# Performance work log

Hardware: AMD Instinct MI355X
Metric: run time of the kernel (lower is better)

## Reference

```python
import jax, jax.numpy as jnp
from jax import lax
import numpy as np

EMBED = 256; MDIM = 256; DSTATE = 128; DCONV = 4
NHEADS = 8; HEADDIM = 64; DINNER = 512            # expand=2 -> d_inner=512; headdim 64 -> 8 heads
CONVDIM = DINNER + 2 * DSTATE                      # 768: conv runs over x,B,C channels
DINPROJ = 2 * DINNER + 2 * DSTATE + NHEADS         # 1288
B = 4; H = 64; W = 64; L = H * W

def _ln(x, g, b, eps=1e-5):
    mu = x.mean(-1, keepdims=True)
    v = ((x - mu) ** 2).mean(-1, keepdims=True)
    return (x - mu) / jnp.sqrt(v + eps) * g + b

def _bn(x, g, b, m, v, eps=1e-5):  # x: (B,C,H,W); eval-mode BatchNorm2d
    return (x - m[:, None, None]) / jnp.sqrt(v[:, None, None] + eps) * g[:, None, None] + b[:, None, None]

def _mamba_branch(seq, ln_g, ln_b, in_W, in_b, cw, cb, A_log, Dh, dt_bias, norm_g, out_W, out_b):
    # Pre-LN Mamba2 block with residual. seq: (B, L, MDIM)
    bsz, slen, _ = seq.shape
    x = _ln(seq, ln_g, ln_b)
    zxbcdt = x @ in_W.T + in_b                                   # (B,L,DINPROJ)
    z = zxbcdt[..., :DINNER]
    xBC = zxbcdt[..., DINNER:DINNER + CONVDIM]
    dt = zxbcdt[..., DINNER + CONVDIM:]                          # (B,L,NHEADS)
    # depthwise causal conv1d over sequence dim
    xc = lax.conv_general_dilated(xBC.transpose(0, 2, 1), cw[:, None, :], (1,),
                                  [(DCONV - 1, 0)], feature_group_count=CONVDIM)
    xBC = jax.nn.silu(xc.transpose(0, 2, 1) + cb)
    xh = xBC[..., :DINNER].reshape(bsz, slen, NHEADS, HEADDIM)
    Bm = xBC[..., DINNER:DINNER + DSTATE]                        # (B,L,N)
    Cm = xBC[..., DINNER + DSTATE:]                              # (B,L,N)
    dt = jax.nn.softplus(dt + dt_bias)                           # (B,L,H)
    dA = jnp.exp(dt * (-jnp.exp(A_log)))                         # (B,L,H)
    dtx = dt[..., None] * xh                                     # (B,L,H,P)
    def step(h, inp):
        dA_t, dtx_t, B_t, C_t = inp
        h = h * dA_t[:, :, None, None] + dtx_t[..., None] * B_t[:, None, None, :]
        return h, jnp.einsum('bhpn,bn->bhp', h, C_t)
    h0 = jnp.zeros((bsz, NHEADS, HEADDIM, DSTATE), seq.dtype)
    xs = (dA.transpose(1, 0, 2), dtx.transpose(1, 0, 2, 3),
          Bm.transpose(1, 0, 2), Cm.transpose(1, 0, 2))
    _, ys = lax.scan(step, h0, xs)                               # (L,B,H,P)
    y = ys.transpose(1, 0, 2, 3) + Dh[None, None, :, None] * xh
    y = y.reshape(bsz, slen, DINNER) * jax.nn.silu(z)            # gate
    y = y / jnp.sqrt((y ** 2).mean(-1, keepdims=True) + 1e-5) * norm_g  # RMSNormGated
    return seq + (y @ out_W.T + out_b)

def _forward(curr_bev, prev_bev, conv3_w, bn3_g, bn3_b, bn3_m, bn3_v, conv1_w, bn1_g, bn1_b, bn1_m, bn1_v, fuse_W, fuse_b, ln_g, ln_b, inp_W, inp_b, m_ln_g, m_ln_b, m_in_W, m_in_b, conv_w, conv_b, A_log, Dp, dt_bias, m_norm_g, m_out_W, m_out_b, outp_W, outp_b, bev_h, bev_w):
    b, l, c = curr_bev.shape
    curr = curr_bev.reshape(b, bev_h, bev_w, c)
    prev = prev_bev.reshape(b, bev_h, bev_w, c)  # delta_yaw is None -> no alignment
    cat = jnp.concatenate([curr, prev], -1).transpose(0, 3, 1, 2)         # (B,2C,H,W)
    b3 = _bn(lax.conv_general_dilated(cat, conv3_w, (1, 1), [(1, 1), (1, 1)]), bn3_g, bn3_b, bn3_m, bn3_v)
    b1 = _bn(lax.conv_general_dilated(cat, conv1_w, (1, 1), [(0, 0), (0, 0)]), bn1_g, bn1_b, bn1_m, bn1_v)
    z = jax.nn.relu(jnp.concatenate([b3, b1], 1)).transpose(0, 2, 3, 1)   # (B,H,W,C)
    z = _ln(z @ fuse_W.T + fuse_b, ln_g, ln_b)
    fl = z.reshape(b, l, c)                                               # row-major forward
    fu = z.transpose(0, 2, 1, 3).reshape(b, l, c)                         # column-major forward
    seqs = jnp.stack([fl, fu, fl[:, ::-1], fu[:, ::-1]], 0)               # (4,B,L,C)
    def branch(seq, iW, ib, lg, lb, mW, mb, cw, cb, al, dh, db, ng, oW, ob, pW, pb):
        s = seq @ iW.T + ib
        s = _mamba_branch(s, lg, lb, mW, mb, cw, cb, al, dh, db, ng, oW, ob)
        return s @ pW.T + pb
    outs = jax.vmap(branch)(seqs, inp_W, inp_b, m_ln_g, m_ln_b, m_in_W, m_in_b, conv_w, conv_b, A_log, Dp, dt_bias, m_norm_g, m_out_W, m_out_b, outp_W, outp_b)
    ofl = outs[0].reshape(b, bev_h, bev_w, c)
    ofu = outs[1].reshape(b, bev_w, bev_h, c).transpose(0, 2, 1, 3)
    orl = outs[2][:, ::-1].reshape(b, bev_h, bev_w, c)
    oru = outs[3][:, ::-1].reshape(b, bev_w, bev_h, c).transpose(0, 2, 1, 3)
    fused = 0.25 * (ofl + ofu + orl + oru)
    return curr_bev + fused.reshape(b, l, c)  # resid dropout = identity at inference

def setup_inputs() -> dict:
    key = jax.random.key(0)
    ks = jax.random.split(key, 16)
    rn = lambda k, s, sc=0.02: jax.random.normal(k, s, jnp.float32) * sc
    return {
        "curr_bev": jax.random.normal(ks[0], (B, L, EMBED), jnp.float32),
        "prev_bev": jax.random.normal(ks[1], (B, L, EMBED), jnp.float32),
        "conv3_w": rn(ks[2], (EMBED // 2, 2 * EMBED, 3, 3)),
        "bn3_g": jnp.ones((EMBED // 2,)), "bn3_b": jnp.zeros((EMBED // 2,)),
        "bn3_m": jnp.zeros((EMBED // 2,)), "bn3_v": jnp.ones((EMBED // 2,)),
        "conv1_w": rn(ks[3], (EMBED // 2, 2 * EMBED, 1, 1)),
        "bn1_g": jnp.ones((EMBED // 2,)), "bn1_b": jnp.zeros((EMBED // 2,)),
        "bn1_m": jnp.zeros((EMBED // 2,)), "bn1_v": jnp.ones((EMBED // 2,)),
        "fuse_W": rn(ks[4], (EMBED, EMBED)), "fuse_b": jnp.zeros((EMBED,)),
        "ln_g": jnp.ones((EMBED,)), "ln_b": jnp.zeros((EMBED,)),
        "inp_W": rn(ks[5], (4, MDIM, EMBED)), "inp_b": jnp.zeros((4, MDIM)),
        "m_ln_g": jnp.ones((4, MDIM)), "m_ln_b": jnp.zeros((4, MDIM)),
        "m_in_W": rn(ks[6], (4, DINPROJ, MDIM)), "m_in_b": jnp.zeros((4, DINPROJ)),
        "conv_w": rn(ks[7], (4, CONVDIM, DCONV), 0.1), "conv_b": jnp.zeros((4, CONVDIM)),
        "A_log": jnp.tile(jnp.log(jnp.arange(1, NHEADS + 1, dtype=jnp.float32)), (4, 1)),
        "Dp": jnp.ones((4, NHEADS)),
        "dt_bias": rn(ks[8], (4, NHEADS), 0.1),
        "m_norm_g": jnp.ones((4, DINNER)),
        "m_out_W": rn(ks[9], (4, MDIM, DINNER)), "m_out_b": jnp.zeros((4, MDIM)),
        "outp_W": rn(ks[10], (4, EMBED, MDIM)), "outp_b": jnp.zeros((4, EMBED)),
        "bev_h": H, "bev_w": W,
    }

def reference(curr_bev, prev_bev, conv3_w, bn3_g, bn3_b, bn3_m, bn3_v, conv1_w, bn1_g, bn1_b, bn1_m, bn1_v, fuse_W, fuse_b, ln_g, ln_b, inp_W, inp_b, m_ln_g, m_ln_b, m_in_W, m_in_b, conv_w, conv_b, A_log, Dp, dt_bias, m_norm_g, m_out_W, m_out_b, outp_W, outp_b, bev_h, bev_w):
    return _forward(curr_bev, prev_bev, conv3_w, bn3_g, bn3_b, bn3_m, bn3_v, conv1_w, bn1_g, bn1_b, bn1_m, bn1_v, fuse_W, fuse_b, ln_g, ln_b, inp_W, inp_b, m_ln_g, m_ln_b, m_in_W, m_in_b, conv_w, conv_b, A_log, Dp, dt_bias, m_norm_g, m_out_W, m_out_b, outp_W, outp_b, bev_h, bev_w)
```

## Files before the change

kernel.cpp:

```cpp
#include <hip/hip_runtime.h>
#include <hip/hip_bf16.h>
#include <cstdint>
#include <cstddef>

typedef unsigned short u16;
typedef unsigned int u32;
typedef __attribute__((ext_vector_type(8))) __bf16 bfx8;
typedef __attribute__((ext_vector_type(4))) float f32x4;

static __device__ __forceinline__ float bitf(u32 v){ float f; __builtin_memcpy(&f,&v,4); return f; }
static __device__ __forceinline__ float bf2f(u16 v){ return bitf(((u32)v)<<16); }
static __device__ __forceinline__ u16 f2bf(float f){ __bf16 b=(__bf16)f; u16 r; __builtin_memcpy(&r,&b,2); return r; }
static __device__ __forceinline__ u32 pk2(float a,float b){ return (u32)f2bf(a) | ((u32)f2bf(b)<<16); }
static __device__ __forceinline__ void unpk8(uint4 r, float* o){
  o[0]=bitf(r.x<<16); o[1]=bitf(r.x&0xffff0000u);
  o[2]=bitf(r.y<<16); o[3]=bitf(r.y&0xffff0000u);
  o[4]=bitf(r.z<<16); o[5]=bitf(r.z&0xffff0000u);
  o[6]=bitf(r.w<<16); o[7]=bitf(r.w&0xffff0000u);
}
static __device__ __forceinline__ void unpk4(uint2 r, float* o){
  o[0]=bitf(r.x<<16); o[1]=bitf(r.x&0xffff0000u);
  o[2]=bitf(r.y<<16); o[3]=bitf(r.y&0xffff0000u);
}
static __device__ __forceinline__ void async16(void* lds, const void* g){
  __builtin_amdgcn_global_load_lds((const __attribute__((address_space(1))) u32*)g,
                                   (__attribute__((address_space(3))) u32*)lds, 16, 0, 0);
}

struct GemmArgs {
  const u16* A; long aZ; int lda;
  const u16* Bw; long bZ; int ldb;
  const float* bias; int biasZ;
  const float* scale; const float* shift;
  const u16* add; long addZ;
  u16* C; long cZ; int ldc; int colOff;
  int K;
  const u16* pad;
  int dirBase;
};

template<int AMODE, int EPI>
__global__ __launch_bounds__(256)
void gemm_bt(GemmArgs g)
{
  __shared__ u16 smA[128*64];
  __shared__ u16 smB[128*64];
  const int tid = threadIdx.x;
  const int l = tid & 63;
  const int wv = tid >> 6;
  const int wr = wv >> 1, wc = wv & 1;
  const int z = blockIdx.z;
  const int r0 = blockIdx.x * 128;
  const int n0 = blockIdx.y * 128;

  const u16* Abase = g.A + (size_t)z * g.aZ;
  const u16* Bbase = g.Bw + (size_t)z * g.bZ;
  const int ldb = g.ldb ? g.ldb : g.K;

  f32x4 acc[4][4];
  #pragma unroll
  for (int i=0;i<4;i++)
    #pragma unroll
    for (int j=0;j<4;j++) acc[i][j] = (f32x4){0.f,0.f,0.f,0.f};

  const int nkt = g.K >> 6;
  #pragma unroll 1
  for (int kt=0; kt<nkt; ++kt) {
    const int k0 = kt << 6;
    #pragma unroll
    for (int it=0; it<4; ++it) {
      const int s = it*256 + tid;
      const int row = s >> 3, ch = s & 7;
      const u16* ga;
      if (AMODE == 0) {
        ga = Abase + (size_t)(r0+row) * g.lda + k0 + ch*8;
      } else if (AMODE == 1) {
        int rr = r0 + row; int li = rr & 4095; int bb = rr >> 12;
        int dir = g.dirBase + z;
        int l2 = (dir & 2) ? (4095 - li) : li;
        int sl = (dir & 1) ? (((l2 & 63) << 6) | (l2 >> 6)) : l2;
        ga = Abase + (size_t)((bb << 12) | sl) * g.lda + k0 + ch*8;
      } else if (AMODE == 2) {
        int rr = r0 + row; int bb = rr >> 12; int li = rr & 4095;
        int yy = li >> 6, xx = li & 63;
        int tap = z, kin = k0;
        int dy = tap / 3 - 1, dx = tap % 3 - 1;
        ga = g.pad + (((size_t)(bb*66 + yy+dy+1))*66 + (xx+dx+1))*512 + kin + ch*8;
      } else {
        int rr = r0 + row; int bb = rr >> 12; int li = rr & 4095;
        int yy = li >> 6, xx = li & 63;
        ga = g.pad + (((size_t)(bb*66 + yy+1))*66 + (xx+1))*512 + k0 + ch*8;
      }
      async16(&smA[(size_t)(it*256 + (tid & ~63))*8], ga);
      const u16* gb = Bbase + (size_t)(n0+row) * ldb + k0 + ch*8;
      async16(&smB[(size_t)(it*256 + (tid & ~63))*8], gb);
    }
    __syncthreads();
    #pragma unroll
    for (int kk=0; kk<2; ++kk) {
      bfx8 av[4], bv[4];
      #pragma unroll
      for (int mi=0; mi<4; ++mi) {
        int ra = wr*64 + mi*16 + (l & 15);
        av[mi] = *(const bfx8*)&smA[ra*64 + kk*32 + (l>>4)*8];
      }
      #pragma unroll
      for (int ni=0; ni<4; ++ni) {
        int rb = wc*64 + ni*16 + (l & 15);
        bv[ni] = *(const bfx8*)&smB[rb*64 + kk*32 + (l>>4)*8];
      }
      #pragma unroll
      for (int mi=0; mi<4; ++mi)
        #pragma unroll
        for (int ni=0; ni<4; ++ni)
          acc[mi][ni] = __builtin_amdgcn_mfma_f32_16x16x32_bf16(av[mi], bv[ni], acc[mi][ni], 0, 0, 0);
    }
    __syncthreads();
  }

  const float* bias_d = (EPI == 0 || EPI == 3) ? g.bias + (size_t)z * g.biasZ : nullptr;
  const u16* add_d = (EPI == 3) ? g.add + (size_t)z * g.addZ : nullptr;
  u16* Cd = g.C + (size_t)z * g.cZ;
  float* Cf = (float*)g.C + (size_t)z * g.cZ;
  #pragma unroll
  for (int mi=0; mi<4; ++mi) {
    #pragma unroll
    for (int ni=0; ni<4; ++ni) {
      f32x4 v = acc[mi][ni];
      const int gr = r0 + wr*64 + mi*16 + ((l >> 4) << 2);
      const int gc = n0 + wc*64 + ni*16 + (l & 15);
      #pragma unroll
      for (int q=0; q<4; ++q) {
        const int r = gr + q;
        float x = v[q];
        if (EPI == 2) {
          x = fmaxf(fmaf(x, g.scale[gc], g.shift[gc]), 0.f);
          Cd[(size_t)r * g.ldc + g.colOff + gc] = f2bf(x);
        } else if (EPI == 3) {
          x += bias_d[gc] + bf2f(add_d[(size_t)r * g.ldc + gc]);
          Cd[(size_t)r * g.ldc + g.colOff + gc] = f2bf(x);
        } else if (EPI == 4) {
          Cf[(size_t)r * g.ldc + g.colOff + gc] = x;
        } else {
          x += bias_d[gc];
          Cd[(size_t)r * g.ldc + g.colOff + gc] = f2bf(x);
        }
      }
    }
  }
}

__global__ void castk(const float* __restrict__ s, u16* __restrict__ d, int n)
{
  int i = (blockIdx.x*256 + threadIdx.x)*4;
  if (i < n){
    float4 v = *(const float4*)(s+i);
    ushort4 o; o.x=f2bf(v.x); o.y=f2bf(v.y); o.z=f2bf(v.z); o.w=f2bf(v.w);
    *(ushort4*)(d+i) = o;
  }
}

__global__ void c3rep(const float* __restrict__ w, u16* __restrict__ o)
{
  int id = blockIdx.x*256 + threadIdx.x;
  int oc = id / 4608, rem = id % 4608;
  int tap = rem >> 9, ic = rem & 511;
  o[id] = f2bf(w[((size_t)oc*512 + ic)*9 + tap]);
}

__global__ void bnssk(const float* g3,const float* b3,const float* m3,const float* v3,
                      const float* g1,const float* b1,const float* m1,const float* v1,
                      float* out)
{
  int t = threadIdx.x; int i = t & 127;
  if (t < 128){ float sc = g3[i]*rsqrtf(v3[i]+1e-5f); out[i]=sc; out[128+i]=b3[i]-m3[i]*sc; }
  else        { float sc = g1[i]*rsqrtf(v1[i]+1e-5f); out[256+i]=sc; out[384+i]=b1[i]-m1[i]*sc; }
}

__global__ __launch_bounds__(256)
void c3red(const float* __restrict__ P, const float* __restrict__ bnss, u16* __restrict__ zin)
{
  const int id = blockIdx.x*256 + threadIdx.x;
  const size_t base = (size_t)id * 4;
  const int r = (int)(base >> 7), c = (int)(base & 127);
  float4 s = {0.f,0.f,0.f,0.f};
  #pragma unroll
  for (int z=0; z<9; ++z){
    float4 v = *(const float4*)(P + (size_t)z*2097152 + base);
    s.x += v.x; s.y += v.y; s.z += v.z; s.w += v.w;
  }
  float4 sc = *(const float4*)(bnss + c);
  float4 sh = *(const float4*)(bnss + 128 + c);
  ushort4 o;
  o.x = f2bf(fmaxf(fmaf(s.x, sc.x, sh.x), 0.f));
  o.y = f2bf(fmaxf(fmaf(s.y, sc.y, sh.y), 0.f));
  o.z = f2bf(fmaxf(fmaf(s.z, sc.z, sh.z), 0.f));
  o.w = f2bf(fmaxf(fmaf(s.w, sc.w, sh.w), 0.f));
  *(ushort4*)(zin + (size_t)r*256 + c) = o;
}

__global__ __launch_bounds__(256)
void padk(const float* __restrict__ curr, const float* __restrict__ prev, u16* __restrict__ pad)
{
  const int id = blockIdx.x*256 + threadIdx.x;
  const int c8 = id & 63;
  int t = id >> 6;
  const int xx = t % 66; t /= 66;
  const int yy = t % 66; const int b = t / 66;
  const int c0 = c8*8;
  uint4 o;
  if (yy==0 || yy==65 || xx==0 || xx==65){ o.x=0;o.y=0;o.z=0;o.w=0; }
  else {
    const int l = (yy-1)*64 + (xx-1);
    const float* s = (c0 < 256) ? curr + ((size_t)b*4096 + l)*256 + c0
                                : prev + ((size_t)b*4096 + l)*256 + (c0-256);
    float4 a = *(const float4*)s, bb = *(const float4*)(s+4);
    o.x = pk2(a.x,a.y); o.y = pk2(a.z,a.w); o.z = pk2(bb.x,bb.y); o.w = pk2(bb.z,bb.w);
  }
  *(uint4*)(pad + (((size_t)b*66 + yy)*66 + xx)*512 + c0) = o;
}

__global__ __launch_bounds__(256)
void ln256(const u16* __restrict__ in, long inZ, u16* __restrict__ out, long outZ,
           const float* __restrict__ gw, const float* __restrict__ bw, int pz)
{
  const int z = blockIdx.z;
  const int row = blockIdx.x*4 + (threadIdx.x>>6);
  const int l = threadIdx.x & 63;
  const u16* ip = in + (size_t)z*inZ + (size_t)row*256 + l*4;
  ushort4 rr = *(const ushort4*)ip;
  float v0=bf2f(rr.x), v1=bf2f(rr.y), v2=bf2f(rr.z), v3=bf2f(rr.w);
  float s = v0+v1+v2+v3;
  float ss = v0*v0+v1*v1+v2*v2+v3*v3;
  #pragma unroll
  for(int m=1;m<64;m<<=1){ s += __shfl_xor(s,m); ss += __shfl_xor(ss,m); }
  float mu = s*(1.f/256.f);
  float var = ss*(1.f/256.f) - mu*mu;
  float rs = rsqrtf(var + 1e-5f);
  const float* g = gw + (size_t)z*pz; const float* b = bw + (size_t)z*pz;
  int c = l*4;
  u16* op = out + (size_t)z*outZ + (size_t)row*256 + c;
  ushort4 o; o.x=f2bf((v0-mu)*rs*g[c]+b[c]); o.y=f2bf((v1-mu)*rs*g[c+1]+b[c+1]);
  o.z=f2bf((v2-mu)*rs*g[c+2]+b[c+2]); o.w=f2bf((v3-mu)*rs*g[c+3]+b[c+3]);
  *(ushort4*)op = o;
}

__global__ __launch_bounds__(256)
void rms512(u16* __restrict__ Y, const float* __restrict__ gw)
{
  const int z = blockIdx.z;
  const int row = blockIdx.x*4 + (threadIdx.x>>6);
  const int l = threadIdx.x & 63;
  u16* p = Y + ((size_t)z*16384 + row)*512 + l*8;
  uint4 raw = *(const uint4*)p;
  float v[8]; unpk8(raw, v);
  float ss = 0.f;
  #pragma unroll
  for (int j=0;j<8;j++) ss += v[j]*v[j];
  #pragma unroll
  for (int m=1;m<64;m<<=1) ss += __shfl_xor(ss, m);
  const float sc = rsqrtf(ss*(1.f/512.f) + 1e-5f);
  const float* g = gw + (size_t)z*512 + l*8;
  uint4 o;
  o.x = pk2(v[0]*sc*g[0], v[1]*sc*g[1]);
  o.y = pk2(v[2]*sc*g[2], v[3]*sc*g[3]);
  o.z = pk2(v[4]*sc*g[4], v[5]*sc*g[5]);
  o.w = pk2(v[6]*sc*g[6], v[7]*sc*g[7]);
  *(uint4*)p = o;
}

__global__ __launch_bounds__(256)
void dtk(const u16* __restrict__ xln, const float* __restrict__ minW,
         const float* __restrict__ minB, const float* __restrict__ dtb,
         float* __restrict__ DT)
{
  __shared__ float sx[32*257];
  const int z = blockIdx.z;
  const int r0 = blockIdx.x * 32;
  const int tid = threadIdx.x;
  {
    const int rr = tid >> 3, cc = (tid & 7) * 32;
    const u16* src = xln + ((size_t)z*16384 + r0 + rr)*256 + cc;
    #pragma unroll
    for (int q=0;q<4;q++){
      uint4 raw = *(const uint4*)(src + q*8);
      float v[8]; unpk8(raw, v);
      #pragma unroll
      for (int j=0;j<8;j++) sx[rr*257 + cc + q*8 + j] = v[j];
    }
  }
  __syncthreads();
  const int ri = tid >> 3, hv = tid & 7;
  const float* wrow = minW + ((size_t)z*1288 + 1280 + hv)*256;
  float acc = 0.f;
  #pragma unroll 4
  for (int k=0; k<256; k+=4){
    float4 wq = *(const float4*)(wrow + k);
    acc += sx[ri*257+k]*wq.x + sx[ri*257+k+1]*wq.y + sx[ri*257+k+2]*wq.z + sx[ri*257+k+3]*wq.w;
  }
  acc += minB[(size_t)z*1288 + 1280 + hv] + dtb[z*8 + hv];
  float dt = (acc > 20.f) ? acc : log1pf(expf(acc));
  DT[((size_t)z*16384 + r0 + ri)*8 + hv] = dt;
}

__global__ __launch_bounds__(256)
void cak(const float* __restrict__ DT, float* __restrict__ CA,
         const float* __restrict__ alog, int dirBase)
{
  const int z = blockIdx.z;
  const int gidx = blockIdx.x*4 + (threadIdx.x>>6);
  const int lane = threadIdx.x & 63;
  const int c = gidx & 63, bh = gidx >> 6;
  const int b = bh >> 3, hh = bh & 7;
  const size_t row = (size_t)z*16384 + (size_t)b*4096 + c*64 + lane;
  float x = DT[row*8 + hh];
  #pragma unroll
  for (int m=1;m<64;m<<=1){ float o = __shfl_up(x, m); if (lane >= m) x += o; }
  float eA = expf(alog[(dirBase+z)*8 + hh]);
  CA[row*8 + hh] = -eA * x;
}

__global__ __launch_bounds__(256)
void convbc(const u16* __restrict__ xbcr, u16* __restrict__ bcc,
            const float* __restrict__ cw, const float* __restrict__ cb)
{
  __shared__ float cwS[4][256];
  __shared__ float cbS[256];
  const int tid = threadIdx.x;
  const int id = blockIdx.x*256 + tid;
  const int c8 = id & 31;
  const int r = (id >> 5) & 16383;
  const int d = id >> 19;
  {
    float4 w4 = *(const float4*)(cw + ((size_t)d*768 + 512 + tid)*4);
    cwS[0][tid]=w4.x; cwS[1][tid]=w4.y; cwS[2][tid]=w4.z; cwS[3][tid]=w4.w;
    cbS[tid] = cb[(size_t)d*768 + 512 + tid];
  }
  __syncthreads();
  const int li = r & 4095;
  const int col = 512 + c8*8;
  const u16* base = xbcr + (size_t)d*16777216 + (size_t)(r - li)*768 + col;
  float acc[8];
  #pragma unroll
  for (int j=0;j<8;j++) acc[j] = cbS[c8*8+j];
  #pragma unroll
  for (int tap=0; tap<4; ++tap){
    int lt = li - 3 + tap;
    if (lt >= 0){
      uint4 raw = *(const uint4*)(base + (size_t)lt*768);
      float v[8]; unpk8(raw, v);
      #pragma unroll
      for (int j=0;j<8;j++)
        acc[j] = fmaf(v[j], cwS[tap][c8*8+j], acc[j]);
    }
  }
  uint4 o;
  float s[8];
  #pragma unroll
  for (int j=0;j<8;j++) s[j] = acc[j] / (1.f + __expf(-acc[j]));
  o.x = pk2(s[0],s[1]); o.y = pk2(s[2],s[3]); o.z = pk2(s[4],s[5]); o.w = pk2(s[6],s[7]);
  *(uint4*)(bcc + ((size_t)d*16384 + r)*256 + c8*8) = o;
}

__global__ __launch_bounds__(256)
void convx(const u16* __restrict__ xbcr, u16* __restrict__ xct,
           const float* __restrict__ cw, const float* __restrict__ cb)
{
  __shared__ u16 T[128*72];
  __shared__ float cwX[4][128];
  __shared__ float cbX[128];
  const int bx = blockIdx.x, z = blockIdx.z;
  const int pq = bx & 3, c = (bx>>2) & 63, b = bx >> 8;
  const int tid = threadIdx.x;
  const u16* xb = xbcr + (size_t)z*16777216 + (size_t)b*4096*768;
  if (tid < 128){
    float4 w4 = *(const float4*)(cw + (size_t)z*3072 + (pq*128+tid)*4);
    cwX[0][tid]=w4.x; cwX[1][tid]=w4.y; cwX[2][tid]=w4.z; cwX[3][tid]=w4.w;
    cbX[tid] = cb[z*768 + pq*128 + tid];
  }
  __syncthreads();
  #pragma unroll
  for (int u=0; u<4; ++u){
    int idx = u*256 + tid;
    int s = idx >> 4, seg = idx & 15;
    int li = c*64 + s;
    int col = pq*128 + seg*8;
    float acc[8];
    #pragma unroll
    for (int j=0;j<8;j++) acc[j] = cbX[seg*8+j];
    #pragma unroll
    for (int tap=0; tap<4; ++tap){
      int lt = li - 3 + tap;
      if (lt >= 0){
        uint4 raw = *(const uint4*)(xb + (size_t)lt*768 + col);
        float v[8]; unpk8(raw, v);
        #pragma unroll
        for (int j=0;j<8;j++) acc[j] = fmaf(v[j], cwX[tap][seg*8+j], acc[j]);
      }
    }
    #pragma unroll
    for (int j=0;j<8;j++)
      T[(seg*8+j)*72 + s] = f2bf(acc[j] / (1.f + __expf(-acc[j])));
  }
  __syncthreads();
  #pragma unroll
  for (int u=0; u<4; ++u){
    int idx = u*256 + tid;
    int pl = idx >> 3, sg = idx & 7;
    uint4 v = *(const uint4*)&T[pl*72 + sg*8];
    *(uint4*)(xct + (size_t)z*8388608 + (size_t)(pq*128+pl)*16384 + b*4096 + c*64 + sg*8) = v;
  }
}

__global__ __launch_bounds__(256)
void btk(const u16* __restrict__ bcc, u16* __restrict__ bt)
{
  __shared__ u16 T[128*72];
  const int bx = blockIdx.x, z = blockIdx.z;
  const int c = bx & 63, b = bx >> 6;
  const int tid = threadIdx.x;
  const u16* src = bcc + ((size_t)z*16384 + (size_t)b*4096 + c*64)*256;
  #pragma unroll
  for (int u=0; u<4; ++u){
    int idx = u*256 + tid;
    int s = idx >> 4, seg = idx & 15;
    uint4 raw = *(const uint4*)(src + (size_t)s*256 + seg*8);
    u16 t8[8]; *(uint4*)t8 = raw;
    #pragma unroll
    for (int j=0;j<8;j++) T[(seg*8+j)*72 + s] = t8[j];
  }
  __syncthreads();
  #pragma unroll
  for (int u=0; u<4; ++u){
    int idx = u*256 + tid;
    int n = idx >> 3, sg = idx & 7;
    uint4 v = *(const uint4*)&T[n*72 + sg*8];
    *(uint4*)(bt + (size_t)z*2097152 + (size_t)n*16384 + b*4096 + c*64 + sg*8) = v;
  }
}

__global__ __launch_bounds__(256)
void csk(const u16* __restrict__ xct, const u16* __restrict__ bt,
         const float* __restrict__ DT, const float* __restrict__ CA,
         u16* __restrict__ CS)
{
  __shared__ u16 Xw[128*72];
  __shared__ u16 Bt[128*72];
  __shared__ float wS[64*2];
  const int bx = blockIdx.x, z = blockIdx.z;
  const int pq = bx & 3, c = (bx>>2) & 63, b = bx >> 8;
  const int tid = threadIdx.x, l = tid & 63, w = tid >> 6;
  const size_t rowb = (size_t)z*16384 + (size_t)b*4096;
  const int p0 = pq*128;
  if (tid < 128){
    int s = tid & 63, hi = tid >> 6;
    int hh = pq*2 + hi;
    float ca63 = CA[(rowb + c*64 + 63)*8 + hh];
    float cav  = CA[(rowb + c*64 + s)*8 + hh];
    float dtv  = DT[(rowb + c*64 + s)*8 + hh];
    wS[s*2+hi] = __expf(ca63 - cav) * dtv;
  }
  __syncthreads();
  #pragma unroll
  for (int u=0; u<4; ++u){
    int idx = u*256 + tid;
    int pl = idx >> 3, sg = idx & 7;
    int hi = pl >> 6;
    uint4 raw = *(const uint4*)(xct + (size_t)z*8388608 + (size_t)(p0+pl)*16384 + b*4096 + c*64 + sg*8);
    float v[8]; unpk8(raw, v);
    uint4 o;
    o.x = pk2(v[0]*wS[(sg*8+0)*2+hi], v[1]*wS[(sg*8+1)*2+hi]);
    o.y = pk2(v[2]*wS[(sg*8+2)*2+hi], v[3]*wS[(sg*8+3)*2+hi]);
    o.z = pk2(v[4]*wS[(sg*8+4)*2+hi], v[5]*wS[(sg*8+5)*2+hi]);
    o.w = pk2(v[6]*wS[(sg*8+6)*2+hi], v[7]*wS[(sg*8+7)*2+hi]);
    *(uint4*)&Xw[pl*72 + sg*8] = o;
  }
  #pragma unroll
  for (int u=0; u<4; ++u){
    int idx = u*256 + tid;
    int n = idx >> 3, sg = idx & 7;
    *(uint4*)&Bt[n*72 + sg*8] =
      *(const uint4*)(bt + (size_t)z*2097152 + (size_t)n*16384 + b*4096 + c*64 + sg*8);
  }
  __syncthreads();
  f32x4 acc[8][2];
  #pragma unroll
  for (int i=0;i<8;i++)
    #pragma unroll
    for (int j=0;j<2;j++) acc[i][j] = (f32x4){0.f,0.f,0.f,0.f};
  #pragma unroll
  for (int kk=0; kk<2; ++kk){
    bfx8 bvp[2];
    #pragma unroll
    for (int ni=0; ni<2; ++ni)
      bvp[ni] = *(const bfx8*)&Xw[(w*32 + ni*16 + (l&15))*72 + kk*32 + (l>>4)*8];
    #pragma unroll
    for (int mi=0; mi<8; ++mi){
      bfx8 av = *(const bfx8*)&Bt[(mi*16 + (l&15))*72 + kk*32 + (l>>4)*8];
      #pragma unroll
      for (int ni=0; ni<2; ++ni)
        acc[mi][ni] = __builtin_amdgcn_mfma_f32_16x16x32_bf16(av, bvp[ni], acc[mi][ni], 0, 0, 0);
    }
  }
  #pragma unroll
  for (int mi=0; mi<8; ++mi){
    #pragma unroll
    for (int ni=0; ni<2; ++ni){
      int gp = p0 + w*32 + ni*16 + (l&15);
      int bhx = b*8 + (gp>>6); int pin = gp & 63;
      int n0 = mi*16 + ((l>>4)<<2);
      u32* cp = (u32*)&CS[(size_t)z*16777216 + (size_t)bhx*524288 + (size_t)c*8192 + (size_t)pin*128 + n0];
      cp[0] = pk2(acc[mi][ni][0], acc[mi][ni][1]);
      cp[1] = pk2(acc[mi][ni][2], acc[mi][ni][3]);
    }
  }
}

__global__ __launch_bounds__(256)
void combk(const u16* __restrict__ CS, const float* __restrict__ CA,
           u16* __restrict__ H)
{
  __shared__ float aL[64];
  const int bx = blockIdx.x;
  const int z = blockIdx.z;
  const int nh = bx & 1, pg = (bx >> 1) & 3, bh = bx >> 3;
  const int b = bh >> 3, hh = bh & 7;
  const int tid = threadIdx.x;
  const int p = pg*16 + (tid >> 4), n = nh*64 + (tid & 15)*4;
  const size_t rowb = (size_t)z*16384 + (size_t)b*4096;
  if (tid < 64) aL[tid] = __expf(CA[(rowb + tid*64 + 63)*8 + hh]);
  __syncthreads();
  const u16* Cs = CS + (size_t)z*16777216 + (size_t)bh*524288 + (size_t)p*128 + n;
  u16* Hd = H + (size_t)z*16777216 + (size_t)bh*524288 + (size_t)p*128 + n;
  float h[4];
  #pragma unroll
  for (int j=0;j<4;j++) h[j]=0.f;
  uint2 pf = *(const uint2*)Cs;
  #pragma unroll 1
  for (int c=0; c<64; ++c){
    uint2 cur = pf;
    if (c < 63) pf = *(const uint2*)(Cs + (size_t)(c+1)*8192);
    uint2 o;
    o.x = pk2(h[0],h[1]); o.y = pk2(h[2],h[3]);
    *(uint2*)(Hd + (size_t)c*8192) = o;
    float v[4]; unpk4(cur, v);
    const float a = aL[c];
    #pragma unroll
    for (int j=0;j<4;j++) h[j] = fmaf(h[j], a, v[j]);
  }
}

__global__ __launch_bounds__(256)
void yk2(const u16* __restrict__ bcc, const u16* __restrict__ xct,
         const float* __restrict__ DT, const float* __restrict__ CA,
         const u16* __restrict__ H, const float* __restrict__ Dp,
         u16* __restrict__ Y)
{
  __shared__ u16 Bs[64*136];
  __shared__ u16 Hs[64*136];
  __shared__ u16 Xt[64*72];
  __shared__ u16 Sm[64*72];
  __shared__ float caL[64], dtL[64];
  const int bx = blockIdx.x, z = blockIdx.z;
  const int c = bx & 63, bh = bx >> 6;
  const int b = bh >> 3, hh = bh & 7;
  const int tid = threadIdx.x, l = tid & 63, w = tid >> 6;
  const size_t rowb = (size_t)z*16384 + (size_t)b*4096;
  const u16* bcp = bcc + (rowb + c*64)*256;
  const u16* Hd = H + (size_t)z*16777216 + (size_t)bh*524288 + (size_t)c*8192;
  const u16* xcp = xct + (size_t)z*8388608 + (size_t)(hh*64)*16384 + b*4096 + c*64;
  const float Dh = Dp[z*8 + hh];

  bfx8 av[4];
  #pragma unroll
  for (int kk=0; kk<4; ++kk)
    av[kk] = *(const bfx8*)(bcp + (size_t)(w*16 + (l&15))*256 + 128 + kk*32 + (l>>4)*8);

  if (tid < 64){
    caL[tid] = CA[(rowb + c*64 + tid)*8 + hh];
    dtL[tid] = DT[(rowb + c*64 + tid)*8 + hh];
  }
  #pragma unroll
  for (int u=0; u<4; ++u){
    int idx = u*256 + tid; int s = idx >> 4, sg = idx & 15;
    *(uint4*)&Bs[s*136 + sg*8] = *(const uint4*)(bcp + (size_t)s*256 + sg*8);
  }
  #pragma unroll
  for (int u=0; u<4; ++u){
    int idx = u*256 + tid; int p = idx >> 4, sg = idx & 15;
    *(uint4*)&Hs[p*136 + sg*8] = *(const uint4*)(Hd + (size_t)p*128 + sg*8);
  }
  #pragma unroll
  for (int u=0; u<2; ++u){
    int idx = u*256 + tid; int p = idx >> 3, sg = idx & 7;
    *(uint4*)&Xt[p*72 + sg*8] = *(const uint4*)(xcp + (size_t)p*16384 + sg*8);
  }
  __syncthreads();

  f32x4 sacc[4], acc2[4];
  #pragma unroll
  for (int i=0;i<4;i++){ sacc[i] = (f32x4){0.f,0.f,0.f,0.f}; acc2[i] = (f32x4){0.f,0.f,0.f,0.f}; }
  #pragma unroll
  for (int kk=0; kk<4; ++kk){
    #pragma unroll
    for (int st=0; st<4; ++st){
      bfx8 bv = *(const bfx8*)&Bs[(st*16 + (l&15))*136 + kk*32 + (l>>4)*8];
      sacc[st] = __builtin_amdgcn_mfma_f32_16x16x32_bf16(av[kk], bv, sacc[st], 0, 0, 0);
      bfx8 hv = *(const bfx8*)&Hs[(st*16 + (l&15))*136 + kk*32 + (l>>4)*8];
      acc2[st] = __builtin_amdgcn_mfma_f32_16x16x32_bf16(av[kk], hv, acc2[st], 0, 0, 0);
    }
  }
  #pragma unroll
  for (int st=0; st<4; ++st){
    #pragma unroll
    for (int q=0;q<4;q++){
      int t = w*16 + (l>>4)*4 + q;
      int s = st*16 + (l&15);
      float m = (s <= t) ? __expf(caL[t]-caL[s]) * dtL[s] : 0.f;
      Sm[t*72 + s] = f2bf(sacc[st][q] * m);
    }
  }
  #pragma unroll
  for (int pt=0; pt<4; ++pt)
    #pragma unroll
    for (int q=0;q<4;q++){
      int t = w*16 + (l>>4)*4 + q;
      acc2[pt][q] *= __expf(caL[t]);
    }
  __syncthreads();
  #pragma unroll
  for (int kk=0; kk<2; ++kk){
    bfx8 sv = *(const bfx8*)&Sm[(w*16 + (l&15))*72 + kk*32 + (l>>4)*8];
    #pragma unroll
    for (int pt=0; pt<4; ++pt){
      bfx8 bv = *(const bfx8*)&Xt[(pt*16 + (l&15))*72 + kk*32 + (l>>4)*8];
      acc2[pt] = __builtin_amdgcn_mfma_f32_16x16x32_bf16(sv, bv, acc2[pt], 0, 0, 0);
    }
  }
  u16* Yrow = Y + (rowb + c*64)*512 + hh*64;
  #pragma unroll
  for (int pt=0; pt<4; ++pt){
    #pragma unroll
    for (int q=0;q<4;q++){
      int t = w*16 + (l>>4)*4 + q;
      int p = pt*16 + (l&15);
      float xv = bf2f(Xt[p*72 + t]);
      float zf = bf2f(Yrow[(size_t)t*512 + p]);
      float yv = (acc2[pt][q] + Dh*xv) * (zf/(1.f+__expf(-zf)));
      Yrow[(size_t)t*512 + p] = f2bf(yv);
    }
  }
}

__global__ __launch_bounds__(256)
void finalk(const float* __restrict__ curr, const u16* __restrict__ outs, float* __restrict__ o)
{
  const int row = blockIdx.x*4 + (threadIdx.x>>6);
  const int c4 = (threadIdx.x & 63)*4;
  const int b = row >> 12, li = row & 4095;
  const int T = ((li & 63) << 6) | (li >> 6);
  const size_t rb = (size_t)b*4096;
  const ushort4 a0 = *(const ushort4*)(outs + (size_t)0*4194304 + ((rb+li)*256 + c4));
  const ushort4 a1 = *(const ushort4*)(outs + (size_t)1*4194304 + ((rb+T)*256 + c4));
  const ushort4 a2 = *(const ushort4*)(outs + (size_t)2*4194304 + ((rb+4095-li)*256 + c4));
  const ushort4 a3 = *(const ushort4*)(outs + (size_t)3*4194304 + ((rb+4095-T)*256 + c4));
  float4 cv = *(const float4*)(curr + (size_t)row*256 + c4);
  float4 r;
  r.x = cv.x + 0.25f*(bf2f(a0.x)+bf2f(a1.x)+bf2f(a2.x)+bf2f(a3.x));
  r.y = cv.y + 0.25f*(bf2f(a0.y)+bf2f(a1.y)+bf2f(a2.y)+bf2f(a3.y));
  r.z = cv.z + 0.25f*(bf2f(a0.z)+bf2f(a1.z)+bf2f(a2.z)+bf2f(a3.z));
  r.w = cv.w + 0.25f*(bf2f(a0.w)+bf2f(a1.w)+bf2f(a2.w)+bf2f(a3.w));
  *(float4*)(o + (size_t)row*256 + c4) = r;
}

extern "C" void kernel_launch(void* const* d_in, const int* in_sizes, int n_in,
                              void* d_out, int out_size, void* d_ws, size_t ws_size,
                              hipStream_t stream)
{
  (void)in_sizes; (void)n_in; (void)out_size;
  const float* curr   = (const float*)d_in[0];
  const float* prev   = (const float*)d_in[1];
  const float* conv3w = (const float*)d_in[2];
  const float* bn3g=(const float*)d_in[3], *bn3b=(const float*)d_in[4], *bn3m=(const float*)d_in[5], *bn3v=(const float*)d_in[6];
  const float* conv1w = (const float*)d_in[7];
  const float* bn1g=(const float*)d_in[8], *bn1b=(const float*)d_in[9], *bn1m=(const float*)d_in[10], *bn1v=(const float*)d_in[11];
  const float* fuseW=(const float*)d_in[12], *fuseB=(const float*)d_in[13];
  const float* lng=(const float*)d_in[14], *lnb=(const float*)d_in[15];
  const float* inpW=(const float*)d_in[16], *inpB=(const float*)d_in[17];
  const float* mlng=(const float*)d_in[18], *mlnb=(const float*)d_in[19];
  const float* minW=(const float*)d_in[20], *minB=(const float*)d_in[21];
  const float* cw=(const float*)d_in[22], *cb=(const float*)d_in[23];
  const float* alog=(const float*)d_in[24], *Dp=(const float*)d_in[25], *dtb=(const float*)d_in[26];
  const float* mng=(const float*)d_in[27];
  const float* moutW=(const float*)d_in[28], *moutB=(const float*)d_in[29];
  const float* outpW=(const float*)d_in[30], *outpB=(const float*)d_in[31];

  char* ws = (char*)d_ws;
  size_t off = 0;
  auto alloc = [&](size_t bytes){ size_t o = off; off = (off + bytes + 1023) & ~(size_t)1023; return o; };
  const size_t O_WFUSE = alloc((size_t)256*256*2);
  const size_t O_WINP  = alloc((size_t)4*256*256*2);
  const size_t O_WMIN  = alloc((size_t)4*1288*256*2);
  const size_t O_WMOUT = alloc((size_t)4*256*512*2);
  const size_t O_WOUTP = alloc((size_t)4*256*256*2);
  const size_t O_WC3   = alloc((size_t)128*4608*2);
  const size_t O_WC1   = alloc((size_t)128*512*2);
  const size_t O_BNSS  = alloc(512*4);
  const size_t O_ZF    = alloc((size_t)16384*256*2);
  const size_t O_OUTS  = alloc((size_t)4*16384*256*2);
  const size_t O_P     = off;

  const size_t S0d  = (size_t)16384*256*2;
  const size_t XLNd = (size_t)16384*256*2;
  const size_t Yd   = (size_t)16384*512*2;
  const size_t XCTd = (size_t)512*16384*2;
  const size_t BTd  = (size_t)128*16384*2;
  const size_t DTd  = (size_t)16384*8*4;
  const size_t CAd  = (size_t)16384*8*4;
  const size_t XHd  = (size_t)16777216*2;
  const size_t perdir = S0d + XLNd + Yd + XCTd + BTd + DTd + CAd + XHd;

  const size_t PADsz = (size_t)4*66*66*512*2;
  const size_t CPsz  = (size_t)9*16384*128*4;
  const size_t PREsz = PADsz + CPsz + (size_t)16384*256*2*2 + 4096;

  int nd = 0;
  for (int cand = 4; cand >= 1; cand >>= 1) {
    size_t need = (size_t)cand*perdir; if (need < PREsz) need = PREsz;
    if (O_P + need <= ws_size) { nd = cand; break; }
  }
  if (nd == 0) return;

  #define WP(o) ((u16*)(ws + (o)))
  #define FP(o) ((float*)(ws + (o)))

  const size_t O_PAD = O_P;
  const size_t O_CP  = O_PAD + PADsz;
  const size_t O_ZIN = O_CP + CPsz;
  const size_t O_ZFT = O_ZIN + (size_t)16384*256*2;

  bnssk<<<1, 256, 0, stream>>>(bn3g,bn3b,bn3m,bn3v, bn1g,bn1b,bn1m,bn1v, FP(O_BNSS));
  castk<<<64, 256, 0, stream>>>(fuseW, WP(O_WFUSE), 65536);
  castk<<<256, 256, 0, stream>>>(inpW, WP(O_WINP), 262144);
  castk<<<1288, 256, 0, stream>>>(minW, WP(O_WMIN), 1318912);
  castk<<<512, 256, 0, stream>>>(moutW, WP(O_WMOUT), 524288);
  castk<<<256, 256, 0, stream>>>(outpW, WP(O_WOUTP), 262144);
  castk<<<64, 256, 0, stream>>>(conv1w, WP(O_WC1), 65536);
  c3rep<<<2304, 256, 0, stream>>>(conv3w, WP(O_WC3));
  padk<<<4356, 256, 0, stream>>>(curr, prev, WP(O_PAD));

  GemmArgs a;
  a = {}; a.A = WP(O_PAD); a.pad = WP(O_PAD);
  a.Bw = WP(O_WC3); a.bZ = 512; a.ldb = 4608;
  a.C = WP(O_CP); a.cZ = 2097152; a.ldc = 128; a.colOff = 0; a.K = 512;
  gemm_bt<2,4><<<dim3(128,1,9), 256, 0, stream>>>(a);
  c3red<<<2048, 256, 0, stream>>>(FP(O_CP), FP(O_BNSS), WP(O_ZIN));
  a = {}; a.A = WP(O_PAD); a.pad = WP(O_PAD); a.Bw = WP(O_WC1); a.bZ = 0; a.ldb = 512;
  a.scale = FP(O_BNSS)+256; a.shift = FP(O_BNSS)+384;
  a.C = WP(O_ZIN); a.cZ = 0; a.ldc = 256; a.colOff = 128; a.K = 512;
  gemm_bt<3,2><<<dim3(128,1,1), 256, 0, stream>>>(a);
  a = {}; a.A = WP(O_ZIN); a.aZ = 0; a.lda = 256; a.Bw = WP(O_WFUSE); a.bZ = 0; a.ldb = 256;
  a.bias = fuseB; a.biasZ = 0; a.C = WP(O_ZFT); a.cZ = 0; a.ldc = 256; a.colOff = 0; a.K = 256;
  gemm_bt<0,0><<<dim3(128,2,1), 256, 0, stream>>>(a);
  ln256<<<dim3(4096,1,1), 256, 0, stream>>>(WP(O_ZFT), 0, WP(O_ZF), 0, lng, lnb, 0);

  for (int d0 = 0; d0 < 4; d0 += nd) {
    size_t o = O_P;
    const size_t O_S0  = o; o += (size_t)nd*S0d;
    const size_t O_XLN = o; o += (size_t)nd*XLNd;
    const size_t O_Y   = o; o += (size_t)nd*Yd;
    const size_t O_XCT = o; o += (size_t)nd*XCTd;
    const size_t O_BT  = o; o += (size_t)nd*BTd;
    const size_t O_DT  = o; o += (size_t)nd*DTd;
    const size_t O_CA  = o; o += (size_t)nd*CAd;
    const size_t O_XH  = o;
    const size_t O_BCC = O_XLN;
    const size_t O_S1  = O_XLN;

    a = {}; a.A = WP(O_ZF); a.aZ = 0; a.lda = 256;
    a.Bw = WP(O_WINP) + (size_t)d0*65536; a.bZ = 65536; a.ldb = 256;
    a.bias = inpB + d0*256; a.biasZ = 256;
    a.C = WP(O_S0); a.cZ = 4194304; a.ldc = 256; a.colOff = 0; a.K = 256; a.dirBase = d0;
    gemm_bt<1,0><<<dim3(128,2,nd), 256, 0, stream>>>(a);
    ln256<<<dim3(4096,1,nd), 256, 0, stream>>>(WP(O_S0), 4194304, WP(O_XLN), 4194304,
                                               mlng + d0*256, mlnb + d0*256, 256);
    dtk<<<dim3(512,1,nd), 256, 0, stream>>>(WP(O_XLN), minW + (size_t)d0*329728,
                                            minB + d0*1288, dtb + d0*8, FP(O_DT));
    cak<<<dim3(512,1,nd), 256, 0, stream>>>(FP(O_DT), FP(O_CA), alog, d0);
    a = {}; a.A = WP(O_XLN); a.aZ = 4194304; a.lda = 256;
    a.Bw = WP(O_WMIN) + (size_t)d0*329728; a.bZ = 329728; a.ldb = 256;
    a.bias = minB + d0*1288; a.biasZ = 1288;
    a.C = WP(O_Y); a.cZ = 8388608; a.ldc = 512; a.colOff = 0; a.K = 256;
    gemm_bt<0,0><<<dim3(128,4,nd), 256, 0, stream>>>(a);
    a = {}; a.A = WP(O_XLN); a.aZ = 4194304; a.lda = 256;
    a.Bw = WP(O_WMIN) + (size_t)d0*329728 + (size_t)512*256; a.bZ = 329728; a.ldb = 256;
    a.bias = minB + d0*1288 + 512; a.biasZ = 1288;
    a.C = WP(O_XH); a.cZ = 16777216; a.ldc = 768; a.colOff = 0; a.K = 256;
    gemm_bt<0,0><<<dim3(128,6,nd), 256, 0, stream>>>(a);
    convbc<<<nd*2048, 256, 0, stream>>>(WP(O_XH), WP(O_BCC), cw + d0*3072, cb + d0*768);
    convx<<<dim3(1024,1,nd), 256, 0, stream>>>(WP(O_XH), WP(O_XCT), cw + d0*3072, cb + d0*768);
    btk<<<dim3(256,1,nd), 256, 0, stream>>>(WP(O_BCC), WP(O_BT));
    csk<<<dim3(1024,1,nd), 256, 0, stream>>>(WP(O_XCT), WP(O_BT), FP(O_DT), FP(O_CA), WP(O_XH));
    combk<<<dim3(256,1,nd), 256, 0, stream>>>(WP(O_XH), FP(O_CA), WP(O_XH));
    yk2<<<dim3(2048,1,nd), 256, 0, stream>>>(WP(O_BCC), WP(O_XCT), FP(O_DT), FP(O_CA),
                                             WP(O_XH), Dp + d0*8, WP(O_Y));
    rms512<<<dim3(4096,1,nd), 256, 0, stream>>>(WP(O_Y), mng + d0*512);
    a = {}; a.A = WP(O_Y); a.aZ = 8388608; a.lda = 512;
    a.Bw = WP(O_WMOUT) + (size_t)d0*131072; a.bZ = 131072; a.ldb = 512;
    a.bias = moutB + d0*256; a.biasZ = 256;
    a.add = WP(O_S0); a.addZ = 4194304;
    a.C = WP(O_S1); a.cZ = 4194304; a.ldc = 256; a.colOff = 0; a.K = 512;
    gemm_bt<0,3><<<dim3(128,2,nd), 256, 0, stream>>>(a);
    a = {}; a.A = WP(O_S1); a.aZ = 4194304; a.lda = 256;
    a.Bw = WP(O_WOUTP) + (size_t)d0*65536; a.bZ = 65536; a.ldb = 256;
    a.bias = outpB + d0*256; a.biasZ = 256;
    a.C = WP(O_OUTS) + (size_t)d0*4194304; a.cZ = 4194304; a.ldc = 256; a.colOff = 0; a.K = 256;
    gemm_bt<0,0><<<dim3(128,2,nd), 256, 0, stream>>>(a);
  }

  finalk<<<4096, 256, 0, stream>>>(curr, WP(O_OUTS), (float*)d_out);

  #undef WP
  #undef FP
}
```

Baseline: 730.7 us.

## Fold RMSNorm into out-proj GEMM and precompute C·B scores per chunk

The RMSNorm gain is folded into the bf16 out-projection weights, and the per-row rsqrt scale is applied in a new GEMM epilogue. The norm kernel now only writes one scale per row instead of rewriting the whole Y tensor. Separately, the intra-chunk C·Bᵀ score matrix is computed once per (batch, chunk) in a new kernel, not recomputed for each of the 8 heads inside yk2, which now loads the precomputed scores from memory. This trades redundant MFMA work for an extra kernel launch and global traffic, and the scores are rounded to bf16 before masking.

```diff
diff --git a/kernel.cpp b/kernel.cpp
--- a/kernel.cpp
+++ b/kernel.cpp
@@ -33,6 +33,7 @@
   const float* bias; int biasZ;
   const float* scale; const float* shift;
   const u16* add; long addZ;
+  const float* rowsc; long rowscZ;
   u16* C; long cZ; int ldc; int colOff;
   int K;
   const u16* pad;
@@ -118,8 +119,9 @@
     __syncthreads();
   }
 
-  const float* bias_d = (EPI == 0 || EPI == 3) ? g.bias + (size_t)z * g.biasZ : nullptr;
-  const u16* add_d = (EPI == 3) ? g.add + (size_t)z * g.addZ : nullptr;
+  const float* bias_d = (EPI == 0 || EPI == 3 || EPI == 5) ? g.bias + (size_t)z * g.biasZ : nullptr;
+  const u16* add_d = (EPI == 3 || EPI == 5) ? g.add + (size_t)z * g.addZ : nullptr;
+  const float* rowsc_d = (EPI == 5) ? g.rowsc + (size_t)z * g.rowscZ : nullptr;
   u16* Cd = g.C + (size_t)z * g.cZ;
   float* Cf = (float*)g.C + (size_t)z * g.cZ;
   #pragma unroll
@@ -139,6 +141,9 @@
         } else if (EPI == 3) {
           x += bias_d[gc] + bf2f(add_d[(size_t)r * g.ldc + gc]);
           Cd[(size_t)r * g.ldc + g.colOff + gc] = f2bf(x);
+        } else if (EPI == 5) {
+          x = x * rowsc_d[r] + bias_d[gc] + bf2f(add_d[(size_t)r * g.ldc + gc]);
+          Cd[(size_t)r * g.ldc + g.colOff + gc] = f2bf(x);
         } else if (EPI == 4) {
           Cf[(size_t)r * g.ldc + g.colOff + gc] = x;
         } else {
@@ -158,6 +163,17 @@
     ushort4 o; o.x=f2bf(v.x); o.y=f2bf(v.y); o.z=f2bf(v.z); o.w=f2bf(v.w);
     *(ushort4*)(d+i) = o;
   }
+}
+
+__global__ void castg(const float* __restrict__ s, const float* __restrict__ gw,
+                      u16* __restrict__ d)
+{
+  int i = (blockIdx.x*256 + threadIdx.x)*4;
+  int dd = i >> 17, k = i & 511;
+  float4 v = *(const float4*)(s+i);
+  float4 g4 = *(const float4*)(gw + dd*512 + k);
+  ushort4 o; o.x=f2bf(v.x*g4.x); o.y=f2bf(v.y*g4.y); o.z=f2bf(v.z*g4.z); o.w=f2bf(v.w*g4.w);
+  *(ushort4*)(d+i) = o;
 }
 
 __global__ void c3rep(const float* __restrict__ w, u16* __restrict__ o)
@@ -246,12 +262,12 @@
 }
 
 __global__ __launch_bounds__(256)
-void rms512(u16* __restrict__ Y, const float* __restrict__ gw)
+void rnormk(const u16* __restrict__ Y, float* __restrict__ RS)
 {
   const int z = blockIdx.z;
   const int row = blockIdx.x*4 + (threadIdx.x>>6);
   const int l = threadIdx.x & 63;
-  u16* p = Y + ((size_t)z*16384 + row)*512 + l*8;
+  const u16* p = Y + ((size_t)z*16384 + row)*512 + l*8;
   uint4 raw = *(const uint4*)p;
   float v[8]; unpk8(raw, v);
   float ss = 0.f;
@@ -259,14 +275,7 @@
   for (int j=0;j<8;j++) ss += v[j]*v[j];
   #pragma unroll
   for (int m=1;m<64;m<<=1) ss += __shfl_xor(ss, m);
-  const float sc = rsqrtf(ss*(1.f/512.f) + 1e-5f);
-  const float* g = gw + (size_t)z*512 + l*8;
-  uint4 o;
-  o.x = pk2(v[0]*sc*g[0], v[1]*sc*g[1]);
-  o.y = pk2(v[2]*sc*g[2], v[3]*sc*g[3]);
-  o.z = pk2(v[4]*sc*g[4], v[5]*sc*g[5]);
-  o.w = pk2(v[6]*sc*g[6], v[7]*sc*g[7]);
-  *(uint4*)p = o;
+  if (l == 0) RS[(size_t)z*16384 + row] = rsqrtf(ss*(1.f/512.f) + 1e-5f);
 }
 
 __global__ __launch_bounds__(256)
@@ -436,6 +445,45 @@
     int n = idx >> 3, sg = idx & 7;
     uint4 v = *(const uint4*)&T[n*72 + sg*8];
     *(uint4*)(bt + (size_t)z*2097152 + (size_t)n*16384 + b*4096 + c*64 + sg*8) = v;
+  }
+}
+
+__global__ __launch_bounds__(256)
+void sk(const u16* __restrict__ bcc, u16* __restrict__ SR)
+{
+  __shared__ u16 Bs[64*136];
+  const int bx = blockIdx.x, z = blockIdx.z;
+  const int c = bx & 63, b = bx >> 6;
+  const int tid = threadIdx.x, l = tid & 63, w = tid >> 6;
+  const u16* bcp = bcc + ((size_t)z*16384 + (size_t)b*4096 + c*64)*256;
+  bfx8 av[4];
+  #pragma unroll
+  for (int kk=0; kk<4; ++kk)
+    av[kk] = *(const bfx8*)(bcp + (size_t)(w*16 + (l&15))*256 + 128 + kk*32 + (l>>4)*8);
+  #pragma unroll
+  for (int u=0; u<4; ++u){
+    int idx = u*256 + tid; int s = idx >> 4, sg = idx & 15;
+    *(uint4*)&Bs[s*136 + sg*8] = *(const uint4*)(bcp + (size_t)s*256 + sg*8);
+  }
+  __syncthreads();
+  f32x4 sacc[4];
+  #pragma unroll
+  for (int i=0;i<4;i++) sacc[i] = (f32x4){0.f,0.f,0.f,0.f};
+  #pragma unroll
+  for (int kk=0; kk<4; ++kk)
+    #pragma unroll
+    for (int st=0; st<4; ++st){
+      bfx8 bv = *(const bfx8*)&Bs[(st*16 + (l&15))*136 + kk*32 + (l>>4)*8];
+      sacc[st] = __builtin_amdgcn_mfma_f32_16x16x32_bf16(av[kk], bv, sacc[st], 0, 0, 0);
+    }
+  u16* Sd = SR + ((size_t)z*4 + b)*524288 + (size_t)c*4096;
+  const int t0 = w*16 + ((l>>4)<<2);
+  #pragma unroll
+  for (int st=0; st<4; ++st){
+    int s = st*16 + (l&15);
+    u32* cp = (u32*)&Sd[(size_t)s*64 + t0];
+    cp[0] = pk2(sacc[st][0], sacc[st][1]);
+    cp[1] = pk2(sacc[st][2], sacc[st][3]);
   }
 }
 
@@ -552,11 +600,12 @@
 
 __global__ __launch_bounds__(256)
 void yk2(const u16* __restrict__ bcc, const u16* __restrict__ xct,
+         const u16* __restrict__ SR,
          const float* __restrict__ DT, const float* __restrict__ CA,
          const u16* __restrict__ H, const float* __restrict__ Dp,
          u16* __restrict__ Y)
 {
-  __shared__ u16 Bs[64*136];
+  __shared__ u16 Ss[64*72];
   __shared__ u16 Hs[64*136];
   __shared__ u16 Xt[64*72];
   __shared__ u16 Sm[64*72];
@@ -569,6 +618,7 @@
   const u16* bcp = bcc + (rowb + c*64)*256;
   const u16* Hd = H + (size_t)z*16777216 + (size_t)bh*524288 + (size_t)c*8192;
   const u16* xcp = xct + (size_t)z*8388608 + (size_t)(hh*64)*16384 + b*4096 + c*64;
+  const u16* Sd = SR + ((size_t)z*4 + b)*524288 + (size_t)c*4096;
   const float Dh = Dp[z*8 + hh];
 
   bfx8 av[4];
@@ -581,9 +631,9 @@
     dtL[tid] = DT[(rowb + c*64 + tid)*8 + hh];
   }
   #pragma unroll
-  for (int u=0; u<4; ++u){
-    int idx = u*256 + tid; int s = idx >> 4, sg = idx & 15;
-    *(uint4*)&Bs[s*136 + sg*8] = *(const uint4*)(bcp + (size_t)s*256 + sg*8);
+  for (int u=0; u<2; ++u){
+    int idx = u*256 + tid; int s = idx >> 3, sg = idx & 7;
+    *(uint4*)&Ss[s*72 + sg*8] = *(const uint4*)(Sd + (size_t)s*64 + sg*8);
   }
   #pragma unroll
   for (int u=0; u<4; ++u){
@@ -597,19 +647,16 @@
   }
   __syncthreads();
 
-  f32x4 sacc[4], acc2[4];
-  #pragma unroll
-  for (int i=0;i<4;i++){ sacc[i] = (f32x4){0.f,0.f,0.f,0.f}; acc2[i] = (f32x4){0.f,0.f,0.f,0.f}; }
-  #pragma unroll
-  for (int kk=0; kk<4; ++kk){
+  f32x4 acc2[4];
+  #pragma unroll
+  for (int i=0;i<4;i++) acc2[i] = (f32x4){0.f,0.f,0.f,0.f};
+  #pragma unroll
+  for (int kk=0; kk<4; ++kk)
     #pragma unroll
     for (int st=0; st<4; ++st){
-      bfx8 bv = *(const bfx8*)&Bs[(st*16 + (l&15))*136 + kk*32 + (l>>4)*8];
-      sacc[st] = __builtin_amdgcn_mfma_f32_16x16x32_bf16(av[kk], bv, sacc[st], 0, 0, 0);
       bfx8 hv = *(const bfx8*)&Hs[(st*16 + (l&15))*136 + kk*32 + (l>>4)*8];
       acc2[st] = __builtin_amdgcn_mfma_f32_16x16x32_bf16(av[kk], hv, acc2[st], 0, 0, 0);
     }
-  }
   #pragma unroll
   for (int st=0; st<4; ++st){
     #pragma unroll
@@ -617,7 +664,7 @@
       int t = w*16 + (l>>4)*4 + q;
       int s = st*16 + (l&15);
       float m = (s <= t) ? __expf(caL[t]-caL[s]) * dtL[s] : 0.f;
-      Sm[t*72 + s] = f2bf(sacc[st][q] * m);
+      Sm[t*72 + s] = f2bf(bf2f(Ss[s*72 + t]) * m);
     }
   }
   #pragma unroll
@@ -717,8 +764,10 @@
   const size_t BTd  = (size_t)128*16384*2;
   const size_t DTd  = (size_t)16384*8*4;
   const size_t CAd  = (size_t)16384*8*4;
+  const size_t SRd  = (size_t)4*64*4096*2;
+  const size_t RSd  = (size_t)16384*4;
   const size_t XHd  = (size_t)16777216*2;
-  const size_t perdir = S0d + XLNd + Yd + XCTd + BTd + DTd + CAd + XHd;
+  const size_t perdir = S0d + XLNd + Yd + XCTd + BTd + DTd + CAd + SRd + RSd + XHd;
 
   const size_t PADsz = (size_t)4*66*66*512*2;
   const size_t CPsz  = (size_t)9*16384*128*4;
@@ -743,7 +792,7 @@
   castk<<<64, 256, 0, stream>>>(fuseW, WP(O_WFUSE), 65536);
   castk<<<256, 256, 0, stream>>>(inpW, WP(O_WINP), 262144);
   castk<<<1288, 256, 0, stream>>>(minW, WP(O_WMIN), 1318912);
-  castk<<<512, 256, 0, stream>>>(moutW, WP(O_WMOUT), 524288);
+  castg<<<512, 256, 0, stream>>>(moutW, mng, WP(O_WMOUT));
   castk<<<256, 256, 0, stream>>>(outpW, WP(O_WOUTP), 262144);
   castk<<<64, 256, 0, stream>>>(conv1w, WP(O_WC1), 65536);
   c3rep<<<2304, 256, 0, stream>>>(conv3w, WP(O_WC3));
@@ -773,6 +822,8 @@
     const size_t O_BT  = o; o += (size_t)nd*BTd;
     const size_t O_DT  = o; o += (size_t)nd*DTd;
     const size_t O_CA  = o; o += (size_t)nd*CAd;
+    const size_t O_SR  = o; o += (size_t)nd*SRd;
+    const size_t O_RS  = o; o += (size_t)nd*RSd;
     const size_t O_XH  = o;
     const size_t O_BCC = O_XLN;
     const size_t O_S1  = O_XLN;
@@ -800,17 +851,19 @@
     convbc<<<nd*2048, 256, 0, stream>>>(WP(O_XH), WP(O_BCC), cw + d0*3072, cb + d0*768);
     convx<<<dim3(1024,1,nd), 256, 0, stream>>>(WP(O_XH), WP(O_XCT), cw + d0*3072, cb + d0*768);
     btk<<<dim3(256,1,nd), 256, 0, stream>>>(WP(O_BCC), WP(O_BT));
+    sk<<<dim3(256,1,nd), 256, 0, stream>>>(WP(O_BCC), WP(O_SR));
     csk<<<dim3(1024,1,nd), 256, 0, stream>>>(WP(O_XCT), WP(O_BT), FP(O_DT), FP(O_CA), WP(O_XH));
     combk<<<dim3(256,1,nd), 256, 0, stream>>>(WP(O_XH), FP(O_CA), WP(O_XH));
-    yk2<<<dim3(2048,1,nd), 256, 0, stream>>>(WP(O_BCC), WP(O_XCT), FP(O_DT), FP(O_CA),
-                                             WP(O_XH), Dp + d0*8, WP(O_Y));
-    rms512<<<dim3(4096,1,nd), 256, 0, stream>>>(WP(O_Y), mng + d0*512);
+    yk2<<<dim3(2048,1,nd), 256, 0, stream>>>(WP(O_BCC), WP(O_XCT), WP(O_SR),
+                                             FP(O_DT), FP(O_CA), WP(O_XH), Dp + d0*8, WP(O_Y));
+    rnormk<<<dim3(4096,1,nd), 256, 0, stream>>>(WP(O_Y), FP(O_RS));
     a = {}; a.A = WP(O_Y); a.aZ = 8388608; a.lda = 512;
     a.Bw = WP(O_WMOUT) + (size_t)d0*131072; a.bZ = 131072; a.ldb = 512;
     a.bias = moutB + d0*256; a.biasZ = 256;
     a.add = WP(O_S0); a.addZ = 4194304;
+    a.rowsc = FP(O_RS); a.rowscZ = 16384;
     a.C = WP(O_S1); a.cZ = 4194304; a.ldc = 256; a.colOff = 0; a.K = 512;
-    gemm_bt<0,3><<<dim3(128,2,nd), 256, 0, stream>>>(a);
+    gemm_bt<0,5><<<dim3(128,2,nd), 256, 0, stream>>>(a);
     a = {}; a.A = WP(O_S1); a.aZ = 4194304; a.lda = 256;
     a.Bw = WP(O_WOUTP) + (size_t)d0*65536; a.bZ = 65536; a.ldb = 256;
     a.bias = outpB + d0*256; a.biasZ = 256;
```

After: 729.4 us. Within noise of the previous version (-0.2%).
